# Kernel tuning notes

Measured on AMD Instinct MI355X. Metric: run time of the kernel, lower is better.

The kernel has to match this reference:

```python
import jax, jax.numpy as jnp
import numpy as np

NUM_EXPERTS = 8
EMBED_DIM = 512
NUM_LAYERS = 2
LN_EPS = 1e-5


def _all_pairs_hyperedges(E):
    # static 'all_pairs' strategy: one hyperedge per unordered expert pair
    nodes, edges = [], []
    eid = 0
    for i in range(E):
        for j in range(i + 1, E):
            nodes += [i, j]
            edges += [eid, eid]
            eid += 1
    return np.asarray(nodes, np.int32), np.asarray(edges, np.int32)


def setup_inputs() -> dict:
    key = jax.random.key(0)
    ks = jax.random.split(key, 4)
    B, L, E, D = 8, 1024, NUM_EXPERTS, EMBED_DIM
    nodes, edges = _all_pairs_hyperedges(E)
    return {
        "expert_outputs": jax.random.normal(ks[0], (B, L, E, D), jnp.float32),
        # HypergraphConv: lin has bias=False, conv bias is separate
        "hgnn_w": jax.random.normal(ks[1], (NUM_LAYERS, D, D), jnp.float32) * 0.02,
        "hgnn_b": jnp.zeros((NUM_LAYERS, D), jnp.float32),
        # combiner: Linear(D,D) -> GELU -> LayerNorm(D)
        "comb_w": jax.random.normal(ks[2], (D, D), jnp.float32) * 0.02,
        "comb_b": jnp.zeros((D,), jnp.float32),
        "ln_gamma": jnp.ones((D,), jnp.float32),
        "ln_beta": jnp.zeros((D,), jnp.float32),
        "nodes_idx": jnp.asarray(nodes),
        "edges_idx": jnp.asarray(edges),
    }


def _hypergraph_conv(h, W, b, nodes_idx, edges_idx, num_edges, d_inv, b_inv):
    # h: [N, E, D] with N = B*L token-graphs sharing the static hyperedge structure.
    # PyG HypergraphConv (no attention, unit edge weights):
    #   out = D^{-1} H B^{-1} H^T (h @ W^T) + b
    x = jnp.einsum('ned,fd->nef', h, W)  # lin(x), bias=False
    N, E, D = x.shape
    # node -> hyperedge scatter-add, scaled by inverse hyperedge degree B^{-1}
    m = jnp.zeros((N, num_edges, D), x.dtype)
    m = m.at[:, edges_idx].add(x[:, nodes_idx]) * b_inv[None, :, None]
    # hyperedge -> node scatter-add, scaled by inverse node degree D^{-1}
    out = jnp.zeros((N, E, D), x.dtype)
    out = out.at[:, nodes_idx].add(m[:, edges_idx]) * d_inv[None, :, None]
    return out + b


def reference(expert_outputs, hgnn_w, hgnn_b, comb_w, comb_b, ln_gamma, ln_beta, nodes_idx, edges_idx):
    B, L, E, D = expert_outputs.shape
    num_edges = nodes_idx.shape[0] // 2  # all_pairs: exactly 2 nodes per hyperedge
    # degree normalizations (unit hyperedge weights)
    deg = jnp.zeros((E,), expert_outputs.dtype).at[nodes_idx].add(1.0)
    d_inv = jnp.where(deg > 0, 1.0 / deg, 0.0)
    edeg = jnp.zeros((num_edges,), expert_outputs.dtype).at[edges_idx].add(1.0)
    b_inv = jnp.where(edeg > 0, 1.0 / edeg, 0.0)

    h = expert_outputs.reshape(B * L, E, D)
    for l in range(hgnn_w.shape[0]):
        h = _hypergraph_conv(h, hgnn_w[l], hgnn_b[l], nodes_idx, edges_idx, num_edges, d_inv, b_inv)

    pooled = h.reshape(B, L, E, D).mean(axis=2)  # [B, L, D]
    z = jax.nn.gelu(pooled @ comb_w.T + comb_b, approximate=False)  # torch nn.GELU = exact
    mu = jnp.mean(z, axis=-1, keepdims=True)
    var = jnp.var(z, axis=-1, keepdims=True)
    return (z - mu) / jnp.sqrt(var + LN_EPS) * ln_gamma + ln_beta
```

## Files before the change

kernel.cpp:

```cpp
#include <hip/hip_runtime.h>
#include <hip/hip_bf16.h>
#include <math.h>


#define DD 512
#define NTOK 8192

typedef short s16x8 __attribute__((ext_vector_type(8)));
typedef short s16x4 __attribute__((ext_vector_type(4)));
typedef float f32x4 __attribute__((ext_vector_type(4)));

static __device__ __forceinline__ short f2bf(float x) {
  unsigned u = __builtin_bit_cast(unsigned, x);
  unsigned r = (u + 0x7fffu + ((u >> 16) & 1u)) >> 16;
  return (short)r;
}

static __device__ __forceinline__ void do_cast4(const float* __restrict__ src,
                                                short* __restrict__ dst, int i) {
  int j = i << 2;
  f32x4 v = *(const f32x4*)(src + j);
  s16x4 o;
  o[0] = f2bf(v[0]); o[1] = f2bf(v[1]); o[2] = f2bf(v[2]); o[3] = f2bf(v[3]);
  *(s16x4*)(dst + j) = o;
}

static __device__ __forceinline__ void do_mv(const float* __restrict__ M,
                                             const float* __restrict__ v,
                                             const float* __restrict__ add,
                                             float* __restrict__ outv,
                                             int gtid) {
  int w = gtid >> 6, l = gtid & 63;
  if (w >= DD) return;
  float s = 0.f;
  for (int k = l; k < DD; k += 64) s += M[(size_t)w * DD + k] * v[k];
#pragma unroll
  for (int m = 32; m; m >>= 1) s += __shfl_xor(s, m);
  if (l == 0) outv[w] = s + add[w];
}

__global__ __launch_bounds__(256) void prep1_kernel(
    const float* __restrict__ w1, const float* __restrict__ w2,
    const float* __restrict__ wc, const float* __restrict__ b1,
    const float* __restrict__ b2, const float* __restrict__ x,
    short* __restrict__ w1t, short* __restrict__ w2b, short* __restrict__ wcb,
    float* __restrict__ tmpv, short* __restrict__ g) {
  int b = blockIdx.x, tid = threadIdx.x;
  if (b >= 896) {
    int i0 = (b - 896) * 256 + tid;
#pragma unroll
    for (int j = 0; j < 2; ++j) {
      int ci = i0 + j * 524288;
      int n = ci >> 7;
      int d4 = (ci & 127) << 2;
      const float* p = x + (size_t)n * (8 * DD) + d4;
      f32x4 s = {0.f, 0.f, 0.f, 0.f};
#pragma unroll
      for (int e = 0; e < 8; ++e) s += *(const f32x4*)(p + e * DD);
      s *= 0.125f;
      s16x4 o;
      o[0] = f2bf(s[0]); o[1] = f2bf(s[1]); o[2] = f2bf(s[2]); o[3] = f2bf(s[3]);
      *(s16x4*)(g + (size_t)n * DD + d4) = o;
    }
  } else if (b < 256) {
    __shared__ float t[32][33];
    int bx = b & 15, by = b >> 4;
    int tx = tid & 31, ty8 = tid >> 5;
    int r0 = by * 32, c0 = bx * 32;
#pragma unroll
    for (int j = 0; j < 4; ++j) {
      int r = ty8 * 4 + j;
      t[r][tx] = w1[(size_t)(r0 + r) * DD + c0 + tx];
    }
    __syncthreads();
#pragma unroll
    for (int j = 0; j < 4; ++j) {
      int r = ty8 * 4 + j;
      w1t[(size_t)(c0 + r) * DD + r0 + tx] = f2bf(t[tx][r]);
    }
  } else if (b < 768) {
    int i = (b - 256) * 256 + tid;
    if (i < 65536) do_cast4(w2, w2b, i);
    else           do_cast4(wc, wcb, i - 65536);
  } else {
    do_mv(w2, b1, b2, tmpv, (b - 768) * 256 + tid);
  }
}

static __device__ __forceinline__ void do_wgemm(const short* __restrict__ A,
                                                const short* __restrict__ B,
                                                short* __restrict__ Out,
                                                int b, int tid) {
  int w = tid >> 6, l = tid & 63;
  int lr = l & 15, lg = l >> 4;
  int m0 = (b >> 3) * 64 + w * 16;
  int n0 = (b & 7) * 64;
  f32x4 acc[4] = {};
  const short* ap = A + (size_t)(m0 + lr) * DD + 8 * lg;
  const short* bp = B + (size_t)(n0 + lr) * DD + 8 * lg;
#pragma unroll
  for (int k0 = 0; k0 < DD; k0 += 32) {
    s16x8 a = *(const s16x8*)(ap + k0);
#pragma unroll
    for (int f = 0; f < 4; ++f) {
      s16x8 bb = *(const s16x8*)(bp + (size_t)f * 16 * DD + k0);
      acc[f] = __builtin_amdgcn_mfma_f32_16x16x32_bf16(a, bb, acc[f], 0, 0, 0);
    }
  }
#pragma unroll
  for (int f = 0; f < 4; ++f)
#pragma unroll
    for (int r = 0; r < 4; ++r)
      Out[(size_t)(m0 + lg * 4 + r) * DD + n0 + f * 16 + lr] = f2bf(acc[f][r]);
}

__global__ __launch_bounds__(256) void prep2_kernel(
    const short* __restrict__ w1t, const short* __restrict__ w2b,
    short* __restrict__ w21t, const float* __restrict__ wc,
    const float* __restrict__ tmpv, const float* __restrict__ cb,
    float* __restrict__ cbias) {
  int b = blockIdx.x, tid = threadIdx.x;
  if (b < 64) do_wgemm(w1t, w2b, w21t, b, tid);
  else        do_mv(wc, tmpv, cb, cbias, (b - 64) * 256 + tid);
}

__global__ __launch_bounds__(256) void prep3_kernel(const short* __restrict__ wcb,
                                                    const short* __restrict__ w21t,
                                                    short* __restrict__ wcomb) {
  do_wgemm(wcb, w21t, wcomb, blockIdx.x, threadIdx.x);
}

__global__ __launch_bounds__(512, 4) void gemm_ln_kernel(
    const short* __restrict__ g, const short* __restrict__ wcomb,
    const float* __restrict__ cbias, const float* __restrict__ gamma,
    const float* __restrict__ beta, float* __restrict__ out) {
  __shared__ short As[16 * DD];
  __shared__ float red[16][8][2];
  int tid = threadIdx.x;
  int w = tid >> 6, l = tid & 63;
  int lr = l & 15, lg = l >> 4;
  int m0 = blockIdx.x * 16;

  {
    const char* gs = (const char*)(g + (size_t)m0 * DD);
    char* ls = (char*)As;
#pragma unroll
    for (int j = 0; j < 2; ++j) {
      int ci = tid + 512 * j;
      int row = ci >> 6;
      int bo = (ci & 63) << 4;
      s16x8 v = *(const s16x8*)(gs + row * 1024 + bo);
      *(s16x8*)(ls + row * 1024 + (bo ^ ((row & 7) << 4))) = v;
    }
  }
  __syncthreads();

  f32x4 acc[4] = {};
  const short* bbase = wcomb + (size_t)(w * 64 + lr) * DD + 8 * lg;
  const char* lsc = (const char*)As;
  for (int k0 = 0; k0 < DD; k0 += 32) {
    int kb = (k0 + 8 * lg) * 2;
    s16x8 a = *(const s16x8*)(lsc + lr * 1024 + (kb ^ ((lr & 7) << 4)));
#pragma unroll
    for (int f = 0; f < 4; ++f) {
      s16x8 b = *(const s16x8*)(bbase + (size_t)f * 16 * DD + k0);
      acc[f] = __builtin_amdgcn_mfma_f32_16x16x32_bf16(a, b, acc[f], 0, 0, 0);
    }
  }

  int cbase = w * 64 + lr;
  float s1[4] = {}, s2[4] = {};
#pragma unroll
  for (int f = 0; f < 4; ++f) {
    float cb = cbias[cbase + f * 16];
#pragma unroll
    for (int r = 0; r < 4; ++r) {
      float xx = acc[f][r] + cb;
      float z = 0.5f * xx * (1.0f + erff(xx * 0.70710678118f));
      acc[f][r] = z;
      s1[r] += z;
      s2[r] += z * z;
    }
  }
#pragma unroll
  for (int m = 1; m < 16; m <<= 1)
#pragma unroll
    for (int r = 0; r < 4; ++r) {
      s1[r] += __shfl_xor(s1[r], m);
      s2[r] += __shfl_xor(s2[r], m);
    }
  if (lr == 0) {
#pragma unroll
    for (int r = 0; r < 4; ++r) {
      int row = lg * 4 + r;
      red[row][w][0] = s1[r];
      red[row][w][1] = s2[r];
    }
  }
  __syncthreads();
#pragma unroll
  for (int r = 0; r < 4; ++r) {
    int row = lg * 4 + r;
    float t1 = 0.f, t2 = 0.f;
#pragma unroll
    for (int ww = 0; ww < 8; ++ww) {
      t1 += red[row][ww][0];
      t2 += red[row][ww][1];
    }
    float mu = t1 * (1.0f / 512.0f);
    float var = t2 * (1.0f / 512.0f) - mu * mu;
    float rs = rsqrtf(var + 1e-5f);
    float* op = out + (size_t)(m0 + row) * DD;
#pragma unroll
    for (int f = 0; f < 4; ++f) {
      int c = cbase + f * 16;
      op[c] = (acc[f][r] - mu) * rs * gamma[c] + beta[c];
    }
  }
}

extern "C" void kernel_launch(void* const* d_in, const int* in_sizes, int n_in,
                              void* d_out, int out_size, void* d_ws, size_t ws_size,
                              hipStream_t stream) {
  const float* x   = (const float*)d_in[0];
  const float* hw  = (const float*)d_in[1];
  const float* hb  = (const float*)d_in[2];
  const float* cw  = (const float*)d_in[3];
  const float* cb  = (const float*)d_in[4];
  const float* gam = (const float*)d_in[5];
  const float* bet = (const float*)d_in[6];
  float* out = (float*)d_out;

  char* ws = (char*)d_ws;
  short* g     = (short*)ws; ws += (size_t)NTOK * DD * 2;
  short* w1t   = (short*)ws; ws += DD * DD * 2;
  short* w2b   = (short*)ws; ws += DD * DD * 2;
  short* wcb   = (short*)ws; ws += DD * DD * 2;
  short* w21t  = (short*)ws; ws += DD * DD * 2;
  short* wcomb = (short*)ws; ws += DD * DD * 2;
  float* tmpv  = (float*)ws; ws += DD * 4;
  float* cbias = (float*)ws; ws += DD * 4;

  const float* W1 = hw;
  const float* W2 = hw + DD * DD;
  const float* b1 = hb;
  const float* b2 = hb + DD;

  prep1_kernel<<<2944, 256, 0, stream>>>(W1, W2, cw, b1, b2, x,
                                         w1t, w2b, wcb, tmpv, g);
  prep2_kernel<<<192, 256, 0, stream>>>(w1t, w2b, w21t, cw, tmpv, cb, cbias);
  prep3_kernel<<<64, 256, 0, stream>>>(wcb, w21t, wcomb);
  gemm_ln_kernel<<<NTOK / 16, 512, 0, stream>>>(g, wcomb, cbias, gam, bet, out);
}
```

Before: 265.1 us.

## Enlarge GEMM+LayerNorm row tile to 128 tokens per block for weight reuse

```diff
diff --git a/kernel.cpp b/kernel.cpp
--- a/kernel.cpp
+++ b/kernel.cpp
@@ -130,22 +130,22 @@
   do_wgemm(wcb, w21t, wcomb, blockIdx.x, threadIdx.x);
 }
 
-__global__ __launch_bounds__(512, 4) void gemm_ln_kernel(
+__global__ __launch_bounds__(512, 2) void gemm_ln_kernel(
     const short* __restrict__ g, const short* __restrict__ wcomb,
     const float* __restrict__ cbias, const float* __restrict__ gamma,
     const float* __restrict__ beta, float* __restrict__ out) {
-  __shared__ short As[16 * DD];
-  __shared__ float red[16][8][2];
+  __shared__ short As[128 * DD];
+  __shared__ float red[128][8][2];
   int tid = threadIdx.x;
   int w = tid >> 6, l = tid & 63;
   int lr = l & 15, lg = l >> 4;
-  int m0 = blockIdx.x * 16;
+  int m0 = blockIdx.x * 128;
 
   {
     const char* gs = (const char*)(g + (size_t)m0 * DD);
     char* ls = (char*)As;
 #pragma unroll
-    for (int j = 0; j < 2; ++j) {
+    for (int j = 0; j < 16; ++j) {
       int ci = tid + 512 * j;
       int row = ci >> 6;
       int bo = (ci & 63) << 4;
@@ -155,68 +155,84 @@
   }
   __syncthreads();
 
-  f32x4 acc[4] = {};
+  f32x4 acc[8][4] = {};
   const short* bbase = wcomb + (size_t)(w * 64 + lr) * DD + 8 * lg;
   const char* lsc = (const char*)As;
   for (int k0 = 0; k0 < DD; k0 += 32) {
     int kb = (k0 + 8 * lg) * 2;
-    s16x8 a = *(const s16x8*)(lsc + lr * 1024 + (kb ^ ((lr & 7) << 4)));
-#pragma unroll
-    for (int f = 0; f < 4; ++f) {
-      s16x8 b = *(const s16x8*)(bbase + (size_t)f * 16 * DD + k0);
-      acc[f] = __builtin_amdgcn_mfma_f32_16x16x32_bf16(a, b, acc[f], 0, 0, 0);
+    s16x8 bb[4];
+#pragma unroll
+    for (int f = 0; f < 4; ++f)
+      bb[f] = *(const s16x8*)(bbase + (size_t)f * 16 * DD + k0);
+#pragma unroll
+    for (int m = 0; m < 8; ++m) {
+      int row = m * 16 + lr;
+      s16x8 a = *(const s16x8*)(lsc + row * 1024 + (kb ^ ((row & 7) << 4)));
+#pragma unroll
+      for (int f = 0; f < 4; ++f)
+        acc[m][f] = __builtin_amdgcn_mfma_f32_16x16x32_bf16(a, bb[f], acc[m][f], 0, 0, 0);
     }
   }
 
   int cbase = w * 64 + lr;
-  float s1[4] = {}, s2[4] = {};
-#pragma unroll
-  for (int f = 0; f < 4; ++f) {
-    float cb = cbias[cbase + f * 16];
+  float cbv[4];
+#pragma unroll
+  for (int f = 0; f < 4; ++f) cbv[f] = cbias[cbase + f * 16];
+
+  float s1[8][4] = {}, s2[8][4] = {};
+#pragma unroll
+  for (int m = 0; m < 8; ++m)
+#pragma unroll
+    for (int f = 0; f < 4; ++f)
+#pragma unroll
+      for (int r = 0; r < 4; ++r) {
+        float xx = acc[m][f][r] + cbv[f];
+        float z = 0.5f * xx * (1.0f + erff(xx * 0.70710678118f));
+        acc[m][f][r] = z;
+        s1[m][r] += z;
+        s2[m][r] += z * z;
+      }
+#pragma unroll
+  for (int msk = 1; msk < 16; msk <<= 1)
+#pragma unroll
+    for (int m = 0; m < 8; ++m)
+#pragma unroll
+      for (int r = 0; r < 4; ++r) {
+        s1[m][r] += __shfl_xor(s1[m][r], msk);
+        s2[m][r] += __shfl_xor(s2[m][r], msk);
+      }
+  if (lr == 0) {
+#pragma unroll
+    for (int m = 0; m < 8; ++m)
+#pragma unroll
+      for (int r = 0; r < 4; ++r) {
+        int row = m * 16 + lg * 4 + r;
+        red[row][w][0] = s1[m][r];
+        red[row][w][1] = s2[m][r];
+      }
+  }
+  __syncthreads();
+#pragma unroll
+  for (int m = 0; m < 8; ++m)
 #pragma unroll
     for (int r = 0; r < 4; ++r) {
-      float xx = acc[f][r] + cb;
-      float z = 0.5f * xx * (1.0f + erff(xx * 0.70710678118f));
-      acc[f][r] = z;
-      s1[r] += z;
-      s2[r] += z * z;
-    }
-  }
-#pragma unroll
-  for (int m = 1; m < 16; m <<= 1)
-#pragma unroll
-    for (int r = 0; r < 4; ++r) {
-      s1[r] += __shfl_xor(s1[r], m);
-      s2[r] += __shfl_xor(s2[r], m);
-    }
-  if (lr == 0) {
-#pragma unroll
-    for (int r = 0; r < 4; ++r) {
-      int row = lg * 4 + r;
-      red[row][w][0] = s1[r];
-      red[row][w][1] = s2[r];
-    }
-  }
-  __syncthreads();
-#pragma unroll
-  for (int r = 0; r < 4; ++r) {
-    int row = lg * 4 + r;
-    float t1 = 0.f, t2 = 0.f;
-#pragma unroll
-    for (int ww = 0; ww < 8; ++ww) {
-      t1 += red[row][ww][0];
-      t2 += red[row][ww][1];
-    }
-    float mu = t1 * (1.0f / 512.0f);
-    float var = t2 * (1.0f / 512.0f) - mu * mu;
-    float rs = rsqrtf(var + 1e-5f);
-    float* op = out + (size_t)(m0 + row) * DD;
-#pragma unroll
-    for (int f = 0; f < 4; ++f) {
-      int c = cbase + f * 16;
-      op[c] = (acc[f][r] - mu) * rs * gamma[c] + beta[c];
-    }
-  }
+      int row = m * 16 + lg * 4 + r;
+      float t1 = 0.f, t2 = 0.f;
+#pragma unroll
+      for (int ww = 0; ww < 8; ++ww) {
+        t1 += red[row][ww][0];
+        t2 += red[row][ww][1];
+      }
+      float mu = t1 * (1.0f / 512.0f);
+      float var = t2 * (1.0f / 512.0f) - mu * mu;
+      float rs = rsqrtf(var + 1e-5f);
+      float* op = out + (size_t)(m0 + row) * DD;
+#pragma unroll
+      for (int f = 0; f < 4; ++f) {
+        int c = cbase + f * 16;
+        op[c] = (acc[m][f][r] - mu) * rs * gamma[c] + beta[c];
+      }
+    }
 }
 
 extern "C" void kernel_launch(void* const* d_in, const int* in_sizes, int n_in,
@@ -250,5 +266,5 @@
                                          w1t, w2b, wcb, tmpv, g);
   prep2_kernel<<<192, 256, 0, stream>>>(w1t, w2b, w21t, cw, tmpv, cb, cbias);
   prep3_kernel<<<64, 256, 0, stream>>>(wcb, w21t, wcomb);
-  gemm_ln_kernel<<<NTOK / 16, 512, 0, stream>>>(g, wcomb, cbias, gam, bet, out);
-}
+  gemm_ln_kernel<<<64, 512, 0, stream>>>(g, wcomb, cbias, gam, bet, out);
+}
```

Result: slower. 321.8 us (+21.4%).
